# Performance work log

Hardware: AMD Instinct MI355X
Metric: run time of the kernel (lower is better)

The kernel has to match this reference:

```python
import jax, jax.numpy as jnp
import numpy as np

WINDOW_SIZE = 8
NUM_HEADS = 16
KAN_GRID = 5
GRID_MIN, GRID_MAX = -2.0, 2.0


def _relative_position_index(ws: int) -> np.ndarray:
    # Same construction as the Keras __init__: pairwise 2D relative coords -> flat index
    coords = np.stack(np.meshgrid(np.arange(ws), np.arange(ws), indexing='ij'))  # [2,ws,ws]
    flat = coords.reshape(2, -1)                                                 # [2,N]
    rel = flat[:, :, None] - flat[:, None, :]                                    # [2,N,N]
    rel = rel.transpose(1, 2, 0)                                                 # [N,N,2]
    rh = (rel[:, :, 0] + ws - 1) * (2 * ws - 1)
    rw = rel[:, :, 1] + ws - 1
    return (rh + rw).astype(np.int32)                                            # [N,N]

_REL_IDX = _relative_position_index(WINDOW_SIZE)


def setup_inputs() -> dict:
    key = jax.random.key(0)
    ks = jax.random.split(key, 8)
    B, N, C = 512, WINDOW_SIZE * WINDOW_SIZE, 512
    G = KAN_GRID
    s = 0.02
    return {
        'x': jax.random.normal(ks[0], (B, N, C), jnp.float32),
        'Wq': jax.random.normal(ks[1], (C, C), jnp.float32) * s,
        'Wk_base': jax.random.normal(ks[2], (C, C), jnp.float32) * s,
        'Wk_spline': jax.random.normal(ks[3], (C * G, C), jnp.float32) * s,
        'Wv': jax.random.normal(ks[4], (C, C), jnp.float32) * s,
        'Wproj': jax.random.normal(ks[5], (C, C), jnp.float32) * s,
        'bproj': jnp.zeros((C,), jnp.float32),
        'bias_table': jax.random.normal(ks[6], ((2 * WINDOW_SIZE - 1) ** 2, NUM_HEADS), jnp.float32) * s,
    }


def _kan_key(x, W_base, W_spline):
    # FastKAN-style KANLinear: base path = swish(x) @ W_base,
    # spline path = Gaussian-RBF basis over each input channel, linearly combined.
    B, N, C = x.shape
    G = KAN_GRID
    grid = jnp.linspace(GRID_MIN, GRID_MAX, G).astype(x.dtype)          # [G]
    h = (GRID_MAX - GRID_MIN) / (G - 1)
    phi = jnp.exp(-(((x[..., None] - grid) / h) ** 2))                  # [B,N,C,G]
    spline = phi.reshape(B, N, C * G) @ W_spline                        # [B,N,C]
    base = jax.nn.swish(x) @ W_base                                     # [B,N,C]
    return base + spline


def reference(x, Wq, Wk_base, Wk_spline, Wv, Wproj, bproj, bias_table):
    B, N, C = x.shape
    H = NUM_HEADS
    hd = C // H
    scale = hd ** -0.5

    def split_heads(t):  # [B,N,C] -> [B,H,N,hd]
        return t.reshape(B, N, H, hd).transpose(0, 2, 1, 3)

    q = split_heads(x @ Wq)
    k = split_heads(_kan_key(x, Wk_base, Wk_spline))
    v = split_heads(x @ Wv)

    scores = jnp.einsum('bhnd,bhmd->bhnm', q, k) * scale                # [B,H,N,N]
    bias = bias_table[_REL_IDX]                                         # [N,N,H]
    scores = scores + bias.transpose(2, 0, 1)[None]                     # + [1,H,N,N]
    # internal padding mask: input already fills the full window, mask is all-ones -> no-op,
    # kept structurally: mask==0 positions would be set to large negative before softmax.
    attn = jax.nn.softmax(scores, axis=-1)
    ctx = jnp.einsum('bhnm,bhmd->bhnd', attn, v)                        # [B,H,N,hd]
    ctx = ctx.transpose(0, 2, 1, 3).reshape(B, N, C)
    return ctx @ Wproj + bproj
```

## Files before the change

### kernel.cpp

```cpp
#include <hip/hip_runtime.h>
#include <hip/hip_bf16.h>

using bf16 = __bf16;
typedef __bf16 bf16x8 __attribute__((ext_vector_type(8)));
typedef __bf16 bf16x4 __attribute__((ext_vector_type(4)));
typedef float  f32x4  __attribute__((ext_vector_type(4)));

__device__ __forceinline__ void gl2lds16(const bf16* g, bf16* l)
{
    __builtin_amdgcn_global_load_lds(
        (const __attribute__((address_space(1))) unsigned int*)g,
        (__attribute__((address_space(3))) unsigned int*)l,
        16, 0, 0);
}

__global__ void prep(const float* __restrict__ x, bf16* __restrict__ xb,
                     bf16* __restrict__ swb, int n)
{
    int base = (blockIdx.x * 256 + threadIdx.x) * 8;
    if (base >= n) return;
    float4 a = *(const float4*)(x + base);
    float4 b = *(const float4*)(x + base + 4);
    float xs[8] = {a.x, a.y, a.z, a.w, b.x, b.y, b.z, b.w};
    bf16x8 xo, so;
#pragma unroll
    for (int t = 0; t < 8; ++t) {
        xo[t] = (bf16)xs[t];
        so[t] = (bf16)(xs[t] / (1.0f + __expf(-xs[t])));
    }
    *(bf16x8*)(xb  + base) = xo;
    *(bf16x8*)(swb + base) = so;
}

__global__ void transpose_k(const float* __restrict__ W, bf16* __restrict__ Wt,
                            int K, int N, int ldT, int total)
{
    int idx = blockIdx.x * 256 + threadIdx.x;
    if (idx >= total) return;
    int k = idx % K;
    int n = idx / K;
    Wt[(size_t)n * ldT + k] = (bf16)W[(size_t)k * N + n];
}

template<int AMODE, bool BIAS, typename CT>
__global__ __launch_bounds__(512, 4)
void gemm_bt(const bf16* __restrict__ A, const float* __restrict__ X,
             const bf16* __restrict__ Bt, CT* __restrict__ C,
             int M, int K, const float* __restrict__ bias)
{
    __shared__ bf16 As[64 * 32];
    __shared__ bf16 Bs[512 * 32];

    const int tid  = threadIdx.x;
    const int lane = tid & 63;
    const int wave = tid >> 6;
    const int quad = lane >> 4;
    const int l15  = lane & 15;
    const int m0   = blockIdx.x * 64;

    f32x4 acc[4][4] = {};

    for (int kt = 0; kt < K; kt += 32) {
#pragma unroll
        for (int cc = 0; cc < 4; ++cc) {
            const int chunk = cc * 512 + tid;
            const int row   = chunk >> 2;
            const int col8  = (chunk & 3) * 8;
            gl2lds16(Bt + (size_t)row * K + kt + col8, Bs + chunk * 8);
        }
        if (AMODE == 0 || kt < 512) {
            if (tid < 256) {
                const int row  = tid >> 2;
                const int col8 = (tid & 3) * 8;
                const int ld   = (AMODE == 0) ? K : 512;
                gl2lds16(A + (size_t)(m0 + row) * ld + kt + col8, As + tid * 8);
            }
        } else {
            if (tid < 256) {
                const int row  = tid >> 2;
                const int col8 = (tid & 3) * 8;
                const int ks = kt + col8 - 512;
                const int c0 = ks / 5;
                const int r0 = ks - c0 * 5;
                const float* xr = X + (size_t)(m0 + row) * 512 + c0;
                const float x0 = xr[0];
                const float x1 = xr[1];
                const float x2v = xr[(c0 < 510) ? 2 : 1];
                bf16x8 o;
                float xv = x0, xnext = x1;
                int g = r0;
#pragma unroll
                for (int t = 0; t < 8; ++t) {
                    float d = xv - (float)(g - 2);
                    o[t] = (bf16)__expf(-d * d);
                    if (++g == 5) { g = 0; xv = xnext; xnext = x2v; }
                }
                *(bf16x8*)(As + row * 32 + col8) = o;
            }
        }
        __syncthreads();

        bf16x8 af[4], bfr[4];
#pragma unroll
        for (int i = 0; i < 4; ++i)
            af[i] = *(const bf16x8*)(As + (i * 16 + l15) * 32 + quad * 8);
#pragma unroll
        for (int j = 0; j < 4; ++j)
            bfr[j] = *(const bf16x8*)(Bs + (wave * 64 + j * 16 + l15) * 32 + quad * 8);
#pragma unroll
        for (int i = 0; i < 4; ++i)
#pragma unroll
            for (int j = 0; j < 4; ++j)
                acc[i][j] = __builtin_amdgcn_mfma_f32_16x16x32_bf16(af[i], bfr[j], acc[i][j], 0, 0, 0);
        __syncthreads();
    }

#pragma unroll
    for (int i = 0; i < 4; ++i) {
#pragma unroll
        for (int j = 0; j < 4; ++j) {
            const int col = wave * 64 + j * 16 + l15;
            const float bv = BIAS ? bias[col] : 0.0f;
#pragma unroll
            for (int r = 0; r < 4; ++r) {
                const int row = m0 + i * 16 + quad * 4 + r;
                C[(size_t)row * 512 + col] = (CT)(acc[i][j][r] + bv);
            }
        }
    }
}

__global__ __launch_bounds__(256)
void attn_mfma(const bf16* __restrict__ q, const bf16* __restrict__ k,
               const bf16* __restrict__ v, const float* __restrict__ bias_table,
               bf16* __restrict__ ctx)
{
    constexpr int LQ = 40;
    constexpr int LV = 72;
    __shared__ bf16 qs[64 * LQ];
    __shared__ bf16 ks[64 * LQ];
    __shared__ bf16 vsT[32 * LV];
    __shared__ bf16 Pl[4][16 * LV];
    __shared__ float bl[225];

    const int bid  = blockIdx.x;
    const int b    = bid >> 4;
    const int h    = bid & 15;
    const int tid  = threadIdx.x;
    const int lane = tid & 63;
    const int w    = tid >> 6;
    const int quad = lane >> 4;
    const int l15  = lane & 15;

    const int n  = tid >> 2;
    const int d0 = (tid & 3) * 8;
    const size_t gbase = ((size_t)(b * 64 + n)) * 512 + h * 32 + d0;
    {
        bf16x8 rq = *(const bf16x8*)(q + gbase);
        bf16x8 rk = *(const bf16x8*)(k + gbase);
        bf16x8 rv = *(const bf16x8*)(v + gbase);
        *(bf16x8*)(qs + n * LQ + d0) = rq;
        *(bf16x8*)(ks + n * LQ + d0) = rk;
#pragma unroll
        for (int t = 0; t < 8; ++t) vsT[(d0 + t) * LV + n] = rv[t];
    }
    if (tid < 225) bl[tid] = bias_table[tid * 16 + h];
    __syncthreads();

    f32x4 sacc[4] = {};
    {
        bf16x8 aq = *(const bf16x8*)(qs + (w * 16 + l15) * LQ + quad * 8);
#pragma unroll
        for (int j = 0; j < 4; ++j) {
            bf16x8 bk = *(const bf16x8*)(ks + (j * 16 + l15) * LQ + quad * 8);
            sacc[j] = __builtin_amdgcn_mfma_f32_16x16x32_bf16(aq, bk, sacc[j], 0, 0, 0);
        }
    }

    bf16* Pw = Pl[w];
    float inv[4];
    {
        const float scale = 0.17677669529663687f;
#pragma unroll
        for (int r = 0; r < 4; ++r) {
            const int row = w * 16 + quad * 4 + r;
            const int rh = row >> 3, rw = row & 7;
            float pv[4];
            float mx = -1e30f;
#pragma unroll
            for (int j = 0; j < 4; ++j) {
                const int c   = j * 16 + l15;
                const int idx = (rh - (c >> 3) + 7) * 15 + (rw - (c & 7) + 7);
                float s = sacc[j][r] * scale + bl[idx];
                pv[j] = s;
                mx = fmaxf(mx, s);
            }
            mx = fmaxf(mx, __shfl_xor(mx, 1, 64));
            mx = fmaxf(mx, __shfl_xor(mx, 2, 64));
            mx = fmaxf(mx, __shfl_xor(mx, 4, 64));
            mx = fmaxf(mx, __shfl_xor(mx, 8, 64));
            float sum = 0.0f;
#pragma unroll
            for (int j = 0; j < 4; ++j) {
                float e = __expf(pv[j] - mx);
                pv[j] = e;
                sum += e;
            }
            sum += __shfl_xor(sum, 1, 64);
            sum += __shfl_xor(sum, 2, 64);
            sum += __shfl_xor(sum, 4, 64);
            sum += __shfl_xor(sum, 8, 64);
            inv[r] = 1.0f / sum;
#pragma unroll
            for (int j = 0; j < 4; ++j)
                Pw[(quad * 4 + r) * LV + j * 16 + l15] = (bf16)pv[j];
        }
    }

    f32x4 oacc[2] = {};
#pragma unroll
    for (int mc = 0; mc < 2; ++mc) {
        bf16x8 ap = *(const bf16x8*)(Pw + l15 * LV + mc * 32 + quad * 8);
#pragma unroll
        for (int dt = 0; dt < 2; ++dt) {
            bf16x8 bv = *(const bf16x8*)(vsT + (dt * 16 + l15) * LV + mc * 32 + quad * 8);
            oacc[dt] = __builtin_amdgcn_mfma_f32_16x16x32_bf16(ap, bv, oacc[dt], 0, 0, 0);
        }
    }

#pragma unroll
    for (int dt = 0; dt < 2; ++dt)
#pragma unroll
        for (int r = 0; r < 4; ++r)
            qs[(w * 16 + quad * 4 + r) * LQ + dt * 16 + l15] = (bf16)(oacc[dt][r] * inv[r]);

    bf16x8 ov = *(const bf16x8*)(qs + n * LQ + d0);
    *(bf16x8*)(ctx + gbase) = ov;
}

extern "C" void kernel_launch(void* const* d_in, const int* in_sizes, int n_in,
                              void* d_out, int out_size, void* d_ws, size_t ws_size,
                              hipStream_t stream)
{
    const float* x       = (const float*)d_in[0];
    const float* Wq      = (const float*)d_in[1];
    const float* Wk_base = (const float*)d_in[2];
    const float* Wk_spl  = (const float*)d_in[3];
    const float* Wv      = (const float*)d_in[4];
    const float* Wproj   = (const float*)d_in[5];
    const float* bproj   = (const float*)d_in[6];
    const float* btab    = (const float*)d_in[7];

    bf16* ws  = (bf16*)d_ws;
    bf16* wqT = ws;
    bf16* wvT = ws + 262144;
    bf16* wpT = ws + 524288;
    bf16* wkT = ws + 786432;
    bf16* xb  = ws + 2359296;
    bf16* q   = ws + 19136512;
    bf16* kk  = ws + 35913728;
    bf16* swb = (bf16*)d_out;
    bf16* vv  = (bf16*)d_out + 16777216;
    bf16* ctx = q;

    prep<<<8192, 256, 0, stream>>>(x, xb, swb, 16777216);

    transpose_k<<<1024, 256, 0, stream>>>(Wq,      wqT,       512,  512, 512,  262144);
    transpose_k<<<1024, 256, 0, stream>>>(Wv,      wvT,       512,  512, 512,  262144);
    transpose_k<<<1024, 256, 0, stream>>>(Wproj,   wpT,       512,  512, 512,  262144);
    transpose_k<<<1024, 256, 0, stream>>>(Wk_base, wkT,       512,  512, 3072, 262144);
    transpose_k<<<5120, 256, 0, stream>>>(Wk_spl,  wkT + 512, 2560, 512, 3072, 1310720);

    gemm_bt<0, false, bf16><<<512, 512, 0, stream>>>(xb,  nullptr, wqT, q,  32768, 512,  nullptr);
    gemm_bt<2, false, bf16><<<512, 512, 0, stream>>>(swb, x,       wkT, kk, 32768, 3072, nullptr);
    gemm_bt<0, false, bf16><<<512, 512, 0, stream>>>(xb,  nullptr, wvT, vv, 32768, 512,  nullptr);

    attn_mfma<<<8192, 256, 0, stream>>>(q, kk, vv, btab, ctx);

    gemm_bt<0, true, float><<<512, 512, 0, stream>>>(ctx, nullptr, wpT, (float*)d_out, 32768, 512, bproj);
}
```

Before: 419.0 us.

## Double-buffer LDS tiles in gemm_bt to overlap loads with MFMA compute

Splits the GEMM's shared-memory A and B tiles into two buffers and prefetches the next K-tile (async global-to-LDS copies, plus raw x loads for the on-the-fly RBF phi tile) while the current tile is being multiplied. The phi values are computed and written after the MFMAs so their global-load latency is hidden. This removes one barrier per iteration and aims to hide memory latency. In exchange it doubles LDS usage to about 72KB per block, which may reduce occupancy below the launch_bounds target of 4 blocks.

```diff
diff --git a/kernel.cpp b/kernel.cpp
--- a/kernel.cpp
+++ b/kernel.cpp
@@ -48,8 +48,8 @@
              const bf16* __restrict__ Bt, CT* __restrict__ C,
              int M, int K, const float* __restrict__ bias)
 {
-    __shared__ bf16 As[64 * 32];
-    __shared__ bf16 Bs[512 * 32];
+    __shared__ bf16 As0[64 * 32],  As1[64 * 32];
+    __shared__ bf16 Bs0[512 * 32], Bs1[512 * 32];
 
     const int tid  = threadIdx.x;
     const int lane = tid & 63;
@@ -59,8 +59,9 @@
     const int m0   = blockIdx.x * 64;
 
     f32x4 acc[4][4] = {};
-
-    for (int kt = 0; kt < K; kt += 32) {
+    float xr3[3];
+
+    auto stage_b = [&](bf16* Bs, int kt) {
 #pragma unroll
         for (int cc = 0; cc < 4; ++cc) {
             const int chunk = cc * 512 + tid;
@@ -68,38 +69,47 @@
             const int col8  = (chunk & 3) * 8;
             gl2lds16(Bt + (size_t)row * K + kt + col8, Bs + chunk * 8);
         }
-        if (AMODE == 0 || kt < 512) {
-            if (tid < 256) {
-                const int row  = tid >> 2;
-                const int col8 = (tid & 3) * 8;
-                const int ld   = (AMODE == 0) ? K : 512;
-                gl2lds16(A + (size_t)(m0 + row) * ld + kt + col8, As + tid * 8);
+    };
+    auto stage_a_copy = [&](bf16* As, int kt) {
+        if (tid < 256) {
+            const int row  = tid >> 2;
+            const int col8 = (tid & 3) * 8;
+            const int ld   = (AMODE == 0) ? K : 512;
+            gl2lds16(A + (size_t)(m0 + row) * ld + kt + col8, As + tid * 8);
+        }
+    };
+    auto phi_load = [&](int kt) {
+        if (tid < 256) {
+            const int col8 = (tid & 3) * 8;
+            const int ks   = kt + col8 - 512;
+            const int c0   = ks / 5;
+            const int row  = tid >> 2;
+            const float* xr = X + (size_t)(m0 + row) * 512 + c0;
+            xr3[0] = xr[0];
+            xr3[1] = xr[1];
+            xr3[2] = xr[(c0 < 510) ? 2 : 1];
+        }
+    };
+    auto phi_store = [&](bf16* As, int kt) {
+        if (tid < 256) {
+            const int row  = tid >> 2;
+            const int col8 = (tid & 3) * 8;
+            const int ks   = kt + col8 - 512;
+            const int c0   = ks / 5;
+            const int r0   = ks - c0 * 5;
+            bf16x8 o;
+            float xv = xr3[0], xnext = xr3[1];
+            int g = r0;
+#pragma unroll
+            for (int t = 0; t < 8; ++t) {
+                float d = xv - (float)(g - 2);
+                o[t] = (bf16)__expf(-d * d);
+                if (++g == 5) { g = 0; xv = xnext; xnext = xr3[2]; }
             }
-        } else {
-            if (tid < 256) {
-                const int row  = tid >> 2;
-                const int col8 = (tid & 3) * 8;
-                const int ks = kt + col8 - 512;
-                const int c0 = ks / 5;
-                const int r0 = ks - c0 * 5;
-                const float* xr = X + (size_t)(m0 + row) * 512 + c0;
-                const float x0 = xr[0];
-                const float x1 = xr[1];
-                const float x2v = xr[(c0 < 510) ? 2 : 1];
-                bf16x8 o;
-                float xv = x0, xnext = x1;
-                int g = r0;
-#pragma unroll
-                for (int t = 0; t < 8; ++t) {
-                    float d = xv - (float)(g - 2);
-                    o[t] = (bf16)__expf(-d * d);
-                    if (++g == 5) { g = 0; xv = xnext; xnext = x2v; }
-                }
-                *(bf16x8*)(As + row * 32 + col8) = o;
-            }
-        }
-        __syncthreads();
-
+            *(bf16x8*)(As + row * 32 + col8) = o;
+        }
+    };
+    auto compute = [&](const bf16* As, const bf16* Bs) {
         bf16x8 af[4], bfr[4];
 #pragma unroll
         for (int i = 0; i < 4; ++i)
@@ -112,7 +122,30 @@
 #pragma unroll
             for (int j = 0; j < 4; ++j)
                 acc[i][j] = __builtin_amdgcn_mfma_f32_16x16x32_bf16(af[i], bfr[j], acc[i][j], 0, 0, 0);
+    };
+
+    stage_b(Bs0, 0);
+    stage_a_copy(As0, 0);
+    __syncthreads();
+
+    bf16 *Ac = As0, *Bc = Bs0, *Aa = As1, *Ba = Bs1;
+
+    const int NT = K >> 5;
+    for (int t = 0; t < NT; ++t) {
+        const int  kn       = (t + 1) << 5;
+        const bool havenext = (t + 1 < NT);
+        const bool nextphi  = (AMODE == 2) && (kn >= 512);
+        if (havenext) {
+            if (nextphi) phi_load(kn);
+            stage_b(Ba, kn);
+            if (!nextphi) stage_a_copy(Aa, kn);
+        }
+        compute(Ac, Bc);
+        if (havenext && nextphi) phi_store(Aa, kn);
         __syncthreads();
+        bf16* s;
+        s = Ac; Ac = Aa; Aa = s;
+        s = Bc; Bc = Ba; Ba = s;
     }
 
 #pragma unroll
```

After: 421.7 us. Within noise of the previous version (+0.6%).
